# Performance work log

Measured on AMD Instinct MI355X. Metric: run time of the kernel, lower is better.

Reference implementation:

```python
import jax, jax.numpy as jnp
import numpy as np

B, T, E = 4, 2048, 1024
H, D = 8, 128  # num_query_heads, head_dimension (single shared KV head -> MQA)


def sinusoidal_pe(length, dim, dtype=jnp.float32):
    """Standard additive sinusoidal PE table of shape (length, dim)."""
    pos = jnp.arange(length, dtype=jnp.float32)[:, None]            # (L, 1)
    inv_freq = jnp.exp(-jnp.log(jnp.float32(10000.0)) * (jnp.arange(0, dim, 2, dtype=jnp.float32) / dim))
    ang = pos * inv_freq[None, :]                                    # (L, dim//2)
    pe = jnp.zeros((length, dim), dtype=jnp.float32)
    pe = pe.at[:, 0::2].set(jnp.sin(ang)).at[:, 1::2].set(jnp.cos(ang))
    return pe.astype(dtype)


def setup_inputs() -> dict:
    key = jax.random.key(0)
    kx, kq, kk, kv, ko = jax.random.split(key, 5)
    s = 0.02  # weight init scale
    return {
        "x": jax.random.normal(kx, (B, T, E), dtype=jnp.float32),
        "Wq": jax.random.normal(kq, (H * D, E), dtype=jnp.float32) * s,
        "Wk": jax.random.normal(kk, (D, E), dtype=jnp.float32) * s,
        "Wv": jax.random.normal(kv, (D, E), dtype=jnp.float32) * s,
        "Wo": jax.random.normal(ko, (E, H * D), dtype=jnp.float32) * s,
    }


def reference(x, Wq, Wk, Wv, Wo):
    Bv, Tv, Ev = x.shape
    scale = 1.0 / jnp.sqrt(jnp.float32(D)).astype(x.dtype)

    q = (x @ Wq.T).reshape(Bv, Tv, H, D)        # (B, T, H, D)
    k = (x @ Wk.T).reshape(Bv, Tv, 1, D)        # (B, T, 1, D) single KV head
    v = (x @ Wv.T).reshape(Bv, Tv, 1, D)

    # positional_embedding applied along axis -2 (as in (.., seq, dim) layout):
    # for k (B,T,1,D) the -2 axis has length 1 -> adds pe[0];
    # for q after permute (B,H,T,D) the -2 axis is T -> full table.
    k = k + sinusoidal_pe(1, D, k.dtype)        # broadcast over (B, T)

    q = jnp.transpose(q, (0, 2, 1, 3))          # (B, H, T, D)
    k1 = k[:, :, 0, :]                          # (B, T, D) shared KV head
    v1 = v[:, :, 0, :]                          # (B, T, D)

    q = q + sinusoidal_pe(Tv, D, q.dtype)[None, None]

    # MQA SDPA: broadcast single K/V head across H query heads
    scores = jnp.einsum("bhtd,bsd->bhts", q, k1) * scale   # (B, H, T, T)
    causal = jnp.tril(jnp.ones((Tv, Tv), dtype=bool))
    scores = jnp.where(causal[None, None], scores, jnp.finfo(scores.dtype).min)
    probs = jax.nn.softmax(scores, axis=-1)
    attn = jnp.einsum("bhts,bsd->bhtd", probs, v1)          # (B, H, T, D)

    out = jnp.transpose(attn, (0, 2, 1, 3)).reshape(Bv, Tv, H * D)
    return out @ Wo.T                                        # (B, T, E)
```

## Files before the change

### kernel.cpp

```cpp
#include <hip/hip_runtime.h>
#include <hip/hip_bf16.h>
#include <cstdint>
#include <cstddef>

#define B_ 4
#define T_ 2048
#define E_ 1024
#define H_ 8
#define D_ 128

typedef unsigned short u16;
typedef __bf16 bf16x8 __attribute__((ext_vector_type(8)));
typedef float f32x4 __attribute__((ext_vector_type(4)));

#define MFMA16(a, b, c) __builtin_amdgcn_mfma_f32_16x16x32_bf16((a), (b), (c), 0, 0, 0)

#if defined(__has_builtin)
#if __has_builtin(__builtin_amdgcn_global_load_lds)
#define HAVE_GLL 1
#endif
#if __has_builtin(__builtin_amdgcn_exp2f)
#define HAVE_EXP2 1
#endif
#endif

__device__ __forceinline__ void gload_lds16(const u16* g, u16* l) {
#ifdef HAVE_GLL
  __builtin_amdgcn_global_load_lds(
      (const __attribute__((address_space(1))) void*)g,
      (__attribute__((address_space(3))) void*)l, 16, 0, 0);
#else
  int lane = threadIdx.x & 63;
  *(uint4*)(l + lane * 8) = *(const uint4*)(g);
#endif
}

__device__ __forceinline__ float fexp2(float x) {
#ifdef HAVE_EXP2
  return __builtin_amdgcn_exp2f(x);
#else
  return __expf(x * 0.69314718056f);
#endif
}

__device__ __forceinline__ u16 f2bf(float f) {
  union { float f; uint32_t u; } a; a.f = f;
  uint32_t u = a.u;
  uint32_t r = (u + 0x7fffu + ((u >> 16) & 1u)) >> 16;
  return (u16)r;
}

__device__ __forceinline__ uint32_t pkbf(float lo, float hi) {
  uint32_t r;
  asm volatile("v_cvt_pk_bf16_f32 %0, %1, %2" : "=v"(r) : "v"(lo), "v"(hi));
  return r;
}

__device__ __forceinline__ void cvt4(const float* __restrict__ s, u16* __restrict__ d, int i4) {
  float4 v = *(const float4*)(s + (size_t)i4 * 4);
  uint2 o;
  o.x = (uint32_t)f2bf(v.x) | ((uint32_t)f2bf(v.y) << 16);
  o.y = (uint32_t)f2bf(v.z) | ((uint32_t)f2bf(v.w) << 16);
  *(uint2*)(d + (size_t)i4 * 4) = o;
}

__global__ __launch_bounds__(256) void prep_kernel(
    const float* __restrict__ x,  const float* __restrict__ Wq,
    const float* __restrict__ Wk, const float* __restrict__ Wv,
    const float* __restrict__ Wo,
    u16* __restrict__ xbf, u16* __restrict__ Wcat, u16* __restrict__ Wobf,
    float* __restrict__ pe)
{
  int id = blockIdx.x * 256 + threadIdx.x;
  if (id < 2097152) { cvt4(x, xbf, id); return; }
  id -= 2097152;
  if (id < 262144) { cvt4(Wq, Wcat, id); return; }
  id -= 262144;
  if (id < 32768) { cvt4(Wk, Wcat + 1048576, id); return; }
  id -= 32768;
  if (id < 32768) { cvt4(Wv, Wcat + 1179648, id); return; }
  id -= 32768;
  if (id < 262144) { cvt4(Wo, Wobf, id); return; }
  id -= 262144;
  int t = id >> 6, i = id & 63;
  float f = expf(-logf(10000.0f) * (float)i / 64.0f);
  float ang = (float)t * f;
  pe[t * 128 + 2 * i]     = sinf(ang);
  pe[t * 128 + 2 * i + 1] = cosf(ang);
}

template<int MODE>
__global__ __launch_bounds__(256) void gemm_nt(
    const u16* __restrict__ A, const u16* __restrict__ Bm,
    u16* __restrict__ Qb, u16* __restrict__ Kb, u16* __restrict__ VTb,
    const float* __restrict__ pe, float* __restrict__ Cout, int K)
{
  __shared__ u16 Al[128 * 32];
  __shared__ u16 Bl[128 * 32];
  const int t = threadIdx.x;
  const int l = t & 63, w = t >> 6;
  const int wr = w >> 1, wc = w & 1;
  const int bm = blockIdx.x * 128, bn = blockIdx.y * 128;
  const int lr = l & 15, lg = l >> 4;

  const int srow = w * 32 + (l >> 2);
  const int scol = (l & 3) * 8;
  const u16* gA0 = A + (size_t)(bm + srow) * K + scol;
  const u16* gB0 = Bm + (size_t)(bn + srow) * K + scol;
  u16* lA0 = &Al[(w * 32) * 32];
  u16* lA1 = &Al[(w * 32 + 16) * 32];
  u16* lB0 = &Bl[(w * 32) * 32];
  u16* lB1 = &Bl[(w * 32 + 16) * 32];
  const size_t r16 = (size_t)16 * K;

  f32x4 acc[4][4] = {};

  for (int k0 = 0; k0 < K; k0 += 32) {
    gload_lds16(gA0 + k0, lA0);
    gload_lds16(gA0 + r16 + k0, lA1);
    gload_lds16(gB0 + k0, lB0);
    gload_lds16(gB0 + r16 + k0, lB1);
    __syncthreads();
    bf16x8 af[4], bfr[4];
    #pragma unroll
    for (int m = 0; m < 4; ++m)
      af[m] = *(const bf16x8*)(&Al[(wr * 64 + m * 16 + lr) * 32 + lg * 8]);
    #pragma unroll
    for (int n = 0; n < 4; ++n)
      bfr[n] = *(const bf16x8*)(&Bl[(wc * 64 + n * 16 + lr) * 32 + lg * 8]);
    __builtin_amdgcn_s_setprio(1);
    #pragma unroll
    for (int m = 0; m < 4; ++m) {
      #pragma unroll
      for (int n = 0; n < 4; ++n)
        acc[m][n] = MFMA16(af[m], bfr[n], acc[m][n]);
    }
    __builtin_amdgcn_s_setprio(0);
    __syncthreads();
  }

  const float qscale = 0.12752869468f;
  #pragma unroll
  for (int m = 0; m < 4; ++m) {
    #pragma unroll
    for (int n = 0; n < 4; ++n) {
      const int gm0 = bm + wr * 64 + m * 16 + lg * 4;
      const int gn = bn + wc * 64 + n * 16 + lr;
      if constexpr (MODE == 0) {
        const int b = gm0 >> 11, tq0 = gm0 & (T_ - 1);
        if (gn < 1024) {
          int hh = gn >> 7, d = gn & 127;
          #pragma unroll
          for (int r = 0; r < 4; ++r)
            Qb[(((size_t)(b * H_ + hh) * T_ + tq0 + r) << 7) + d] =
                f2bf((acc[m][n][r] + pe[((tq0 + r) << 7) + d]) * qscale);
        } else if (gn < 1152) {
          int d = gn - 1024;
          #pragma unroll
          for (int r = 0; r < 4; ++r)
            Kb[((size_t)(gm0 + r) << 7) + d] = f2bf(acc[m][n][r] + (float)(d & 1));
        } else {
          int d = gn - 1152;
          uint2 pk;
          pk.x = pkbf(acc[m][n][0], acc[m][n][1]);
          pk.y = pkbf(acc[m][n][2], acc[m][n][3]);
          *(uint2*)(VTb + ((size_t)(b * 128 + d) << 11) + tq0) = pk;
        }
      } else {
        #pragma unroll
        for (int r = 0; r < 4; ++r)
          Cout[(size_t)(gm0 + r) * 1024 + gn] = acc[m][n][r];
      }
    }
  }
}

__global__ __launch_bounds__(512) void attn_kernel(
    const u16* __restrict__ Qb, const u16* __restrict__ Kb,
    const u16* __restrict__ VTg, u16* __restrict__ Ob)
{
  __shared__ u16 Kl[2][64 * 128];
  __shared__ u16 VTl[2][128 * 64];
  __shared__ u16 Pl[8 * 16 * 64];
  const int t = threadIdx.x;
  const int l = t & 63, w = t >> 6;
  const int lr = l & 15, lg = l >> 4;
  const int sw = lr & 7;
  const int p = blockIdx.x, b = blockIdx.y;
  const int h = w;
  const int q0A = p * 16, q0B = (127 - p) * 16;
  const int ntA = (q0A + 16 + 63) >> 6, ntB = (q0B + 16 + 63) >> 6;

  auto stage = [&](int kt, int s) {
    #pragma unroll
    for (int c = 0; c < 2; ++c) {
      int n = c * 512 + t;
      {
        int row = n >> 4, ul = n & 15;
        int ug = ul ^ (row & 7);
        gload_lds16(Kb + ((size_t)(b * T_ + kt * 64 + row) << 7) + ug * 8,
                    &Kl[s][(size_t)(c * 512 + w * 64) * 8]);
      }
      {
        int row = n >> 3, ul = n & 7;
        int ug = ul ^ (row & 7);
        gload_lds16(VTg + ((size_t)(b * 128 + row) << 11) + kt * 64 + ug * 8,
                    &VTl[s][(size_t)(c * 512 + w * 64) * 8]);
      }
    }
  };

  const u16* qbA = Qb + (((size_t)(b * H_ + h) * T_ + q0A + lr) << 7);
  const u16* qbB = Qb + (((size_t)(b * H_ + h) * T_ + q0B + lr) << 7);
  bf16x8 qfA[4], qfB[4];
  #pragma unroll
  for (int kc = 0; kc < 4; ++kc) {
    qfA[kc] = *(const bf16x8*)(qbA + kc * 32 + lg * 8);
    qfB[kc] = *(const bf16x8*)(qbB + kc * 32 + lg * 8);
  }

  float mA = -3e38f, mB = -3e38f, lA = 0.f, lB = 0.f;
  f32x4 oA[8] = {}, oB[8] = {};
  u16* pw = &Pl[w * 16 * 64];

  auto process = [&](f32x4 (&s)[4], float& m, float& lsum, f32x4 (&o)[8],
                     int q0F, int kt, bool masked, const u16* vtl) {
    float pv[16];
    float pm = -3e38f;
    if (masked) {
      const int qv = q0F + lr;
      #pragma unroll
      for (int kvf = 0; kvf < 4; ++kvf) {
        #pragma unroll
        for (int r = 0; r < 4; ++r) {
          int kv = kt * 64 + kvf * 16 + lg * 4 + r;
          float sv = (kv <= qv) ? s[kvf][r] : -3e38f;
          pv[kvf * 4 + r] = sv;
          pm = fmaxf(pm, sv);
        }
      }
    } else {
      #pragma unroll
      for (int kvf = 0; kvf < 4; ++kvf) {
        #pragma unroll
        for (int r = 0; r < 4; ++r) {
          float sv = s[kvf][r];
          pv[kvf * 4 + r] = sv;
          pm = fmaxf(pm, sv);
        }
      }
    }
    pm = fmaxf(pm, __shfl_xor(pm, 16));
    pm = fmaxf(pm, __shfl_xor(pm, 32));
    float mn;
    if (__all(pm <= m + 11.5f)) {
      mn = m;
    } else {
      mn = fmaxf(m, pm);
      float corr = fexp2(m - mn);
      lsum *= corr;
      #pragma unroll
      for (int df = 0; df < 8; ++df) {
        #pragma unroll
        for (int r = 0; r < 4; ++r) o[df][r] *= corr;
      }
      m = mn;
    }
    float ps = 0.f;
    #pragma unroll
    for (int i = 0; i < 16; ++i) {
      pv[i] = fexp2(pv[i] - mn);
      ps += pv[i];
    }
    ps += __shfl_xor(ps, 16);
    ps += __shfl_xor(ps, 32);
    lsum += ps;
    #pragma unroll
    for (int kvf = 0; kvf < 4; ++kvf) {
      uint2 pk;
      pk.x = pkbf(pv[kvf * 4 + 0], pv[kvf * 4 + 1]);
      pk.y = pkbf(pv[kvf * 4 + 2], pv[kvf * 4 + 3]);
      int un = ((2 * kvf + (lg >> 1)) ^ sw) * 8 + (lg & 1) * 4;
      *(uint2*)(&pw[lr * 64 + un]) = pk;
    }
    __builtin_amdgcn_s_setprio(1);
    #pragma unroll
    for (int kc = 0; kc < 2; ++kc) {
      bf16x8 pf = *(const bf16x8*)(&pw[lr * 64 + ((4 * kc + lg) ^ sw) * 8]);
      #pragma unroll
      for (int df = 0; df < 8; ++df) {
        bf16x8 vf = *(const bf16x8*)(&vtl[(df * 16 + lr) * 64 + ((4 * kc + lg) ^ sw) * 8]);
        o[df] = MFMA16(vf, pf, o[df]);
      }
    }
    __builtin_amdgcn_s_setprio(0);
  };

  stage(0, 0);
  __syncthreads();

  for (int kt = 0; kt < ntB; ++kt) {
    const int cur = kt & 1;
    if (kt + 1 < ntB) stage(kt + 1, cur ^ 1);

    const bool actA = kt < ntA;
    f32x4 sA[4] = {}, sB[4] = {};
    __builtin_amdgcn_s_setprio(1);
    #pragma unroll
    for (int kvf = 0; kvf < 4; ++kvf) {
      bf16x8 kf[4];
      #pragma unroll
      for (int kc = 0; kc < 4; ++kc)
        kf[kc] = *(const bf16x8*)(&Kl[cur][((kvf * 16 + lr) << 7) + ((4 * kc + lg) ^ sw) * 8]);
      #pragma unroll
      for (int kc = 0; kc < 4; ++kc)
        sB[kvf] = MFMA16(kf[kc], qfB[kc], sB[kvf]);
      if (actA) {
        #pragma unroll
        for (int kc = 0; kc < 4; ++kc)
          sA[kvf] = MFMA16(kf[kc], qfA[kc], sA[kvf]);
      }
    }
    __builtin_amdgcn_s_setprio(0);
    process(sB, mB, lB, oB, q0B, kt, kt * 64 + 63 > q0B, &VTl[cur][0]);
    if (actA) process(sA, mA, lA, oA, q0A, kt, kt * 64 + 63 > q0A, &VTl[cur][0]);
    __syncthreads();
  }

  float rA = 1.0f / lA, rB = 1.0f / lB;
  #pragma unroll
  for (int df = 0; df < 8; ++df) {
    uint2 pk;
    pk.x = pkbf(oB[df][0] * rB, oB[df][1] * rB);
    pk.y = pkbf(oB[df][2] * rB, oB[df][3] * rB);
    *(uint2*)(Ob + ((size_t)(b * T_ + q0B + lr) << 10) + h * 128 + df * 16 + lg * 4) = pk;
    pk.x = pkbf(oA[df][0] * rA, oA[df][1] * rA);
    pk.y = pkbf(oA[df][2] * rA, oA[df][3] * rA);
    *(uint2*)(Ob + ((size_t)(b * T_ + q0A + lr) << 10) + h * 128 + df * 16 + lg * 4) = pk;
  }
}

extern "C" void kernel_launch(void* const* d_in, const int* in_sizes, int n_in,
                              void* d_out, int out_size, void* d_ws, size_t ws_size,
                              hipStream_t stream) {
  const float* x  = (const float*)d_in[0];
  const float* Wq = (const float*)d_in[1];
  const float* Wk = (const float*)d_in[2];
  const float* Wv = (const float*)d_in[3];
  const float* Wo = (const float*)d_in[4];

  char* ws = (char*)d_ws;
  size_t off = 0;
  auto alloc = [&](size_t bytes) {
    char* p = ws + off;
    off += (bytes + 255) & ~(size_t)255;
    return p;
  };
  u16*   xbf  = (u16*)  alloc(8388608ull * 2);
  u16*   Wcat = (u16*)  alloc(1310720ull * 2);
  u16*   Wobf = (u16*)  alloc(1048576ull * 2);
  float* pe   = (float*)alloc(262144ull * 4);
  u16*   Qbuf = (u16*)  alloc(8388608ull * 2);
  u16*   Kbuf = (u16*)  alloc(1048576ull * 2);
  u16*   VTbuf= (u16*)  alloc(1048576ull * 2);
  u16*   Abuf = (u16*)  alloc(8388608ull * 2);

  prep_kernel<<<11008, 256, 0, stream>>>(x, Wq, Wk, Wv, Wo, xbf, Wcat, Wobf, pe);

  gemm_nt<0><<<dim3(64, 10), 256, 0, stream>>>(xbf, Wcat, Qbuf, Kbuf, VTbuf, pe, nullptr, 1024);
  attn_kernel<<<dim3(64, 4), 512, 0, stream>>>(Qbuf, Kbuf, VTbuf, Abuf);
  gemm_nt<1><<<dim3(64, 8), 256, 0, stream>>>(Abuf, Wobf, nullptr, nullptr, nullptr, nullptr,
                                              (float*)d_out, 1024);
}
```

Baseline: 145.6 us.

## Split paired causal attention blocks into one query tile per block, longest first

Attention blocks previously each handled a pair of 16-row query tiles (p and 127-p) for load balance. Now each of 512 blocks handles a single 16-row tile, scheduled from the longest causal range downward. The P scratch buffer is dropped by reusing the current K stage buffer after an added barrier, which frees LDS. The aim is more blocks and higher occupancy, at the cost of one extra __syncthreads per KV tile and of each K/V tile being loaded for half as many query rows.

```diff
diff --git a/kernel.cpp b/kernel.cpp
--- a/kernel.cpp
+++ b/kernel.cpp
@@ -181,15 +181,17 @@
 {
   __shared__ u16 Kl[2][64 * 128];
   __shared__ u16 VTl[2][128 * 64];
-  __shared__ u16 Pl[8 * 16 * 64];
   const int t = threadIdx.x;
   const int l = t & 63, w = t >> 6;
   const int lr = l & 15, lg = l >> 4;
   const int sw = lr & 7;
-  const int p = blockIdx.x, b = blockIdx.y;
+  const int bid = blockIdx.x;
+  const int p = 127 - (bid >> 2);
+  const int b = bid & 3;
   const int h = w;
-  const int q0A = p * 16, q0B = (127 - p) * 16;
-  const int ntA = (q0A + 16 + 63) >> 6, ntB = (q0B + 16 + 63) >> 6;
+  const int q0 = p * 16;
+  const int nt = (q0 + 16 + 63) >> 6;
+  const int qv = q0 + lr;
 
   auto stage = [&](int kt, int s) {
     #pragma unroll
@@ -210,25 +212,41 @@
     }
   };
 
-  const u16* qbA = Qb + (((size_t)(b * H_ + h) * T_ + q0A + lr) << 7);
-  const u16* qbB = Qb + (((size_t)(b * H_ + h) * T_ + q0B + lr) << 7);
-  bf16x8 qfA[4], qfB[4];
+  const u16* qb = Qb + (((size_t)(b * H_ + h) * T_ + qv) << 7);
+  bf16x8 qf[4];
   #pragma unroll
-  for (int kc = 0; kc < 4; ++kc) {
-    qfA[kc] = *(const bf16x8*)(qbA + kc * 32 + lg * 8);
-    qfB[kc] = *(const bf16x8*)(qbB + kc * 32 + lg * 8);
-  }
-
-  float mA = -3e38f, mB = -3e38f, lA = 0.f, lB = 0.f;
-  f32x4 oA[8] = {}, oB[8] = {};
-  u16* pw = &Pl[w * 16 * 64];
-
-  auto process = [&](f32x4 (&s)[4], float& m, float& lsum, f32x4 (&o)[8],
-                     int q0F, int kt, bool masked, const u16* vtl) {
+  for (int kc = 0; kc < 4; ++kc)
+    qf[kc] = *(const bf16x8*)(qb + kc * 32 + lg * 8);
+
+  float m = -3e38f, lsum = 0.f;
+  f32x4 o[8] = {};
+
+  stage(0, 0);
+  __syncthreads();
+
+  for (int kt = 0; kt < nt; ++kt) {
+    const int cur = kt & 1;
+    if (kt + 1 < nt) stage(kt + 1, cur ^ 1);
+
+    f32x4 s[4] = {};
+    __builtin_amdgcn_s_setprio(1);
+    #pragma unroll
+    for (int kvf = 0; kvf < 4; ++kvf) {
+      bf16x8 kf[4];
+      #pragma unroll
+      for (int kc = 0; kc < 4; ++kc)
+        kf[kc] = *(const bf16x8*)(&Kl[cur][((kvf * 16 + lr) << 7) + ((4 * kc + lg) ^ sw) * 8]);
+      #pragma unroll
+      for (int kc = 0; kc < 4; ++kc)
+        s[kvf] = MFMA16(kf[kc], qf[kc], s[kvf]);
+    }
+    __builtin_amdgcn_s_setprio(0);
+    __syncthreads();
+
     float pv[16];
     float pm = -3e38f;
+    const bool masked = kt * 64 + 63 > q0;
     if (masked) {
-      const int qv = q0F + lr;
       #pragma unroll
       for (int kvf = 0; kvf < 4; ++kvf) {
         #pragma unroll
@@ -275,6 +293,8 @@
     ps += __shfl_xor(ps, 16);
     ps += __shfl_xor(ps, 32);
     lsum += ps;
+
+    u16* pw = &Kl[cur][w * 1024];
     #pragma unroll
     for (int kvf = 0; kvf < 4; ++kvf) {
       uint2 pk;
@@ -289,54 +309,21 @@
       bf16x8 pf = *(const bf16x8*)(&pw[lr * 64 + ((4 * kc + lg) ^ sw) * 8]);
       #pragma unroll
       for (int df = 0; df < 8; ++df) {
-        bf16x8 vf = *(const bf16x8*)(&vtl[(df * 16 + lr) * 64 + ((4 * kc + lg) ^ sw) * 8]);
+        bf16x8 vf = *(const bf16x8*)(&VTl[cur][(df * 16 + lr) * 64 + ((4 * kc + lg) ^ sw) * 8]);
         o[df] = MFMA16(vf, pf, o[df]);
       }
     }
     __builtin_amdgcn_s_setprio(0);
-  };
-
-  stage(0, 0);
-  __syncthreads();
-
-  for (int kt = 0; kt < ntB; ++kt) {
-    const int cur = kt & 1;
-    if (kt + 1 < ntB) stage(kt + 1, cur ^ 1);
-
-    const bool actA = kt < ntA;
-    f32x4 sA[4] = {}, sB[4] = {};
-    __builtin_amdgcn_s_setprio(1);
-    #pragma unroll
-    for (int kvf = 0; kvf < 4; ++kvf) {
-      bf16x8 kf[4];
-      #pragma unroll
-      for (int kc = 0; kc < 4; ++kc)
-        kf[kc] = *(const bf16x8*)(&Kl[cur][((kvf * 16 + lr) << 7) + ((4 * kc + lg) ^ sw) * 8]);
-      #pragma unroll
-      for (int kc = 0; kc < 4; ++kc)
-        sB[kvf] = MFMA16(kf[kc], qfB[kc], sB[kvf]);
-      if (actA) {
-        #pragma unroll
-        for (int kc = 0; kc < 4; ++kc)
-          sA[kvf] = MFMA16(kf[kc], qfA[kc], sA[kvf]);
-      }
-    }
-    __builtin_amdgcn_s_setprio(0);
-    process(sB, mB, lB, oB, q0B, kt, kt * 64 + 63 > q0B, &VTl[cur][0]);
-    if (actA) process(sA, mA, lA, oA, q0A, kt, kt * 64 + 63 > q0A, &VTl[cur][0]);
     __syncthreads();
   }
 
-  float rA = 1.0f / lA, rB = 1.0f / lB;
+  float rs = 1.0f / lsum;
   #pragma unroll
   for (int df = 0; df < 8; ++df) {
     uint2 pk;
-    pk.x = pkbf(oB[df][0] * rB, oB[df][1] * rB);
-    pk.y = pkbf(oB[df][2] * rB, oB[df][3] * rB);
-    *(uint2*)(Ob + ((size_t)(b * T_ + q0B + lr) << 10) + h * 128 + df * 16 + lg * 4) = pk;
-    pk.x = pkbf(oA[df][0] * rA, oA[df][1] * rA);
-    pk.y = pkbf(oA[df][2] * rA, oA[df][3] * rA);
-    *(uint2*)(Ob + ((size_t)(b * T_ + q0A + lr) << 10) + h * 128 + df * 16 + lg * 4) = pk;
+    pk.x = pkbf(o[df][0] * rs, o[df][1] * rs);
+    pk.y = pkbf(o[df][2] * rs, o[df][3] * rs);
+    *(uint2*)(Ob + ((size_t)(b * T_ + qv) << 10) + h * 128 + df * 16 + lg * 4) = pk;
   }
 }
 
@@ -368,7 +355,7 @@
   prep_kernel<<<11008, 256, 0, stream>>>(x, Wq, Wk, Wv, Wo, xbf, Wcat, Wobf, pe);
 
   gemm_nt<0><<<dim3(64, 10), 256, 0, stream>>>(xbf, Wcat, Qbuf, Kbuf, VTbuf, pe, nullptr, 1024);
-  attn_kernel<<<dim3(64, 4), 512, 0, stream>>>(Qbuf, Kbuf, VTbuf, Abuf);
+  attn_kernel<<<512, 512, 0, stream>>>(Qbuf, Kbuf, VTbuf, Abuf);
   gemm_nt<1><<<dim3(64, 8), 256, 0, stream>>>(Abuf, Wobf, nullptr, nullptr, nullptr, nullptr,
                                               (float*)d_out, 1024);
 }
```

Result: slower. 154.8 us (+6.3%).
